# Kernel optimization log

Hardware: AMD Instinct MI355X
Metric: run time of the kernel (lower is better)

## Reference

```python
import jax, jax.numpy as jnp
import numpy as np

INP = 64   # inplanes
PLN = 64   # planes
LOC = 64   # loc_planes
EPS = 1e-5


def _linear_init(key, fan_in, fan_out):
    # torch nn.Linear default: U(-1/sqrt(fan_in), 1/sqrt(fan_in)) for W and b
    kw, kb = jax.random.split(key)
    bound = 1.0 / np.sqrt(fan_in)
    W = jax.random.uniform(kw, (fan_in, fan_out), jnp.float32, -bound, bound)
    b = jax.random.uniform(kb, (fan_out,), jnp.float32, -bound, bound)
    return W, b


def setup_inputs() -> dict:
    key = jax.random.key(0)
    ks = jax.random.split(key, 8)
    B, N = 8, 4096
    img_fea = jax.random.normal(ks[0], (B, N, INP), jnp.float32)
    loc_fea = jax.random.normal(ks[1], (B, N, LOC), jnp.float32)
    W11, b11 = _linear_init(ks[2], INP + LOC, INP)
    W12, b12 = _linear_init(ks[3], INP, INP)
    W21, b21 = _linear_init(ks[4], INP + LOC, INP)
    W22, b22 = _linear_init(ks[5], INP, INP * PLN)
    W3, b3 = _linear_init(ks[6], PLN, PLN)
    ln_g = jnp.ones((PLN,), jnp.float32)
    ln_b = jnp.zeros((PLN,), jnp.float32)
    return {
        "img_fea": img_fea, "loc_fea": loc_fea,
        "W11": W11, "b11": b11, "W12": W12, "b12": b12,
        "W21": W21, "b21": b21, "W22": W22, "b22": b22,
        "ln_g": ln_g, "ln_b": ln_b, "W3": W3, "b3": b3,
    }


def reference(img_fea, loc_fea, W11, b11, W12, b12, W21, b21, W22, b22,
              ln_g, ln_b, W3, b3):
    B, N, C = img_fea.shape
    cat_fea = jnp.concatenate([img_fea, loc_fea], axis=2)  # [B,N,INP+LOC]
    # branch 1: per-token input vector
    w11 = jax.nn.relu(cat_fea @ W11 + b11)                 # [B,N,INP]
    w12 = w11 @ W12 + b12                                  # [B,N,INP]
    # branch 2: per-token weight matrix generation
    w21 = jax.nn.relu(cat_fea @ W21 + b21)                 # [B,N,INP]
    w22 = (w21 @ W22 + b22).reshape(B, N, INP, PLN)        # [B,N,INP,PLN]
    # batched tiny matvec: (1,INP) @ (INP,PLN) per token
    x = jnp.einsum('bni,bnio->bno', w12, w22)              # [B,N,PLN]
    # LayerNorm over last dim + ReLU
    mu = jnp.mean(x, axis=-1, keepdims=True)
    var = jnp.mean(jnp.square(x - mu), axis=-1, keepdims=True)
    x = (x - mu) * jax.lax.rsqrt(var + EPS) * ln_g + ln_b
    x = jax.nn.relu(x)
    # final linear (no activation)
    return x @ W3 + b3
```

## Files before the change

kernel.cpp:

```cpp
#include <hip/hip_runtime.h>
#include <cstdint>


typedef __bf16 bf16x4 __attribute__((ext_vector_type(4)));
typedef __bf16 bf16x8 __attribute__((ext_vector_type(8)));
typedef float  f32x4  __attribute__((ext_vector_type(4)));
typedef float  f32x8  __attribute__((ext_vector_type(8)));

#define MFMA16(A, B, C) __builtin_amdgcn_mfma_f32_16x16x32_bf16(A, B, C, 0, 0, 0)

#define OFF_BT22 0
#define OFF_W11  266240
#define OFF_W21  274432
#define OFF_W12  282624
#define OFF_W3   286720

__global__ __launch_bounds__(256) void prep_kernel(
    const float* __restrict__ W22, const float* __restrict__ b22,
    const float* __restrict__ W11, const float* __restrict__ W21,
    const float* __restrict__ W12, const float* __restrict__ W3,
    __bf16* __restrict__ ws)
{
    __shared__ __bf16 T[64][72];
    const int b = blockIdx.x, tid = threadIdx.x;
    const float* src; __bf16* dst;
    if (b < 64)       { src = W22 + b * 4096;        dst = ws + OFF_BT22 + b * 4096; }
    else if (b == 64) { src = b22;                   dst = ws + OFF_BT22 + 64 * 4096; }
    else if (b < 67)  { src = W11 + (b - 65) * 4096; dst = ws + OFF_W11 + (b - 65) * 4096; }
    else if (b < 69)  { src = W21 + (b - 67) * 4096; dst = ws + OFF_W21 + (b - 67) * 4096; }
    else if (b == 69) { src = W12;                   dst = ws + OFF_W12; }
    else              { src = W3;                    dst = ws + OFF_W3; }
    #pragma unroll
    for (int it = 0; it < 4; ++it) {
        int u = it * 1024 + tid * 4;
        int r = u >> 6, c = u & 63;
        const float4 v = *(const float4*)(src + u);
        T[r][c] = (__bf16)v.x; T[r][c + 1] = (__bf16)v.y;
        T[r][c + 2] = (__bf16)v.z; T[r][c + 3] = (__bf16)v.w;
    }
    __syncthreads();
    #pragma unroll
    for (int it = 0; it < 2; ++it) {
        int item = it * 256 + tid;
        int q = item >> 6, o = item & 63;
        bf16x8 pk;
        #pragma unroll
        for (int kj = 0; kj < 8; ++kj) pk[kj] = T[q * 8 + kj][o];
        *(bf16x8*)(dst + q * 512 + o * 8) = pk;
    }
}

__global__ __launch_bounds__(256, 1) void main_kernel(
    const float* __restrict__ img, const float* __restrict__ loc,
    const float* __restrict__ b11, const float* __restrict__ b12,
    const float* __restrict__ b21, const float* __restrict__ ln_g,
    const float* __restrict__ ln_b, const float* __restrict__ b3,
    const __bf16* __restrict__ ws, float* __restrict__ out)
{
    __shared__ __align__(1024) char smem[102400];
    __bf16* catL = (__bf16*)smem;
    __bf16* w11L = (__bf16*)(smem + 34816);
    __bf16* w21L = (__bf16*)(smem + 65536);
    __bf16* w12L = (__bf16*)(smem + 83968);

    const int tid  = threadIdx.x;
    const int wv   = tid >> 6;
    const int lane = tid & 63;
    const int ln   = lane & 15;
    const int quad = lane >> 4;
    const int wt   = wv * 32;
    const long tb  = (long)blockIdx.x * 128;

    const __bf16* Bt22  = ws + OFF_BT22;
    const __bf16* W11bt = ws + OFF_W11;
    const __bf16* W21bt = ws + OFF_W21;
    const __bf16* W12bt = ws + OFF_W12;
    const __bf16* W3bt  = ws + OFF_W3;

    {
        const float* srcs[2] = {img, loc};
        #pragma unroll
        for (int s = 0; s < 2; ++s) {
            const float* src = srcs[s] + tb * 64;
            #pragma unroll
            for (int it = 0; it < 8; ++it) {
                int u = (it * 256 + tid) * 4;
                int t = u >> 6, c = u & 63;
                const float4 v = *(const float4*)(src + u);
                bf16x4 pk = {(__bf16)v.x, (__bf16)v.y, (__bf16)v.z, (__bf16)v.w};
                *(bf16x4*)(catL + t * 136 + s * 64 + c) = pk;
            }
        }
    }
    __syncthreads();

    {
        f32x4 a11[2][4] = {}; f32x4 a21[2][4] = {};
        #pragma unroll
        for (int kb = 0; kb < 4; ++kb) {
            bf16x8 af[2];
            #pragma unroll
            for (int mf = 0; mf < 2; ++mf)
                af[mf] = *(const bf16x8*)(catL + (wt + mf*16 + ln)*136 + kb*32 + quad*8);
            #pragma unroll
            for (int nf = 0; nf < 4; ++nf) {
                int o = nf*16 + ln;
                bf16x8 bw1 = *(const bf16x8*)(W11bt + ((kb*4 + quad)*64 + o)*8);
                bf16x8 bw2 = *(const bf16x8*)(W21bt + ((kb*4 + quad)*64 + o)*8);
                #pragma unroll
                for (int mf = 0; mf < 2; ++mf) {
                    a11[mf][nf] = MFMA16(af[mf], bw1, a11[mf][nf]);
                    a21[mf][nf] = MFMA16(af[mf], bw2, a21[mf][nf]);
                }
            }
        }
        #pragma unroll
        for (int nf = 0; nf < 4; ++nf) {
            int o = nf*16 + ln;
            float c11 = b11[o], c21 = b21[o];
            #pragma unroll
            for (int mf = 0; mf < 2; ++mf)
                #pragma unroll
                for (int r = 0; r < 4; ++r) {
                    int t = wt + mf*16 + quad*4 + r;
                    float v1 = a11[mf][nf][r] + c11; v1 = v1 > 0.f ? v1 : 0.f;
                    float v2 = a21[mf][nf][r] + c21; v2 = v2 > 0.f ? v2 : 0.f;
                    w11L[t*72 + o] = (__bf16)v1;
                    w21L[t*72 + o] = (__bf16)v2;
                }
        }
    }
    __syncthreads();

    auto stage = [&](int c) {
        const int ng = (c == 16) ? 8 : 32;
        char* buf = smem + (c & 1) * 32768;
        for (int g = wv; g < ng; g += 4) {
            const __bf16* gsrc = Bt22 + ((long)c * 16384 + g * 512) + lane * 8;
            void* ldst = buf + g * 1024;
            __builtin_amdgcn_global_load_lds(
                (const __attribute__((address_space(1))) uint32_t*)gsrc,
                (__attribute__((address_space(3))) uint32_t*)ldst, 16, 0, 0);
        }
    };
    stage(0);

    {
        f32x4 a12c[2][4] = {};
        #pragma unroll
        for (int kb = 0; kb < 2; ++kb) {
            bf16x8 af[2];
            #pragma unroll
            for (int mf = 0; mf < 2; ++mf)
                af[mf] = *(const bf16x8*)(w11L + (wt + mf*16 + ln)*72 + kb*32 + quad*8);
            #pragma unroll
            for (int nf = 0; nf < 4; ++nf) {
                bf16x8 bw = *(const bf16x8*)(W12bt + ((kb*4 + quad)*64 + nf*16 + ln)*8);
                #pragma unroll
                for (int mf = 0; mf < 2; ++mf)
                    a12c[mf][nf] = MFMA16(af[mf], bw, a12c[mf][nf]);
            }
        }
        #pragma unroll
        for (int nf = 0; nf < 4; ++nf) {
            int o = nf*16 + ln;
            float c12 = b12[o];
            #pragma unroll
            for (int mf = 0; mf < 2; ++mf)
                #pragma unroll
                for (int r = 0; r < 4; ++r) {
                    int t = wt + mf*16 + quad*4 + r;
                    w12L[t*72 + o] = (__bf16)(a12c[mf][nf][r] + c12);
                }
        }
    }
    __syncthreads();

    bf16x8 a12[2][2]; f32x8 w12f[2][2];
    #pragma unroll
    for (int mf = 0; mf < 2; ++mf)
        #pragma unroll
        for (int sub = 0; sub < 2; ++sub) {
            a12[mf][sub]  = *(const bf16x8*)(w12L + (wt + mf*16 + ln)*72 + sub*32 + quad*8);
            w12f[mf][sub] = __builtin_convertvector(a12[mf][sub], f32x8);
        }

    f32x4 acc[2][4] = {};
    for (int c = 0; c <= 16; ++c) {
        if (c < 16) stage(c + 1);
        const __bf16* buf = (const __bf16*)(smem + (c & 1) * 32768);
        if (c < 16) {
            bf16x4 w21v[2];
            #pragma unroll
            for (int mf = 0; mf < 2; ++mf)
                w21v[mf] = *(const bf16x4*)(w21L + (wt + mf*16 + ln)*72 + c*4);
            #pragma unroll
            for (int s = 0; s < 8; ++s) {
                int sub = s & 1;
                bf16x8 af[2];
                #pragma unroll
                for (int mf = 0; mf < 2; ++mf) {
                    float wj = (float)w21v[mf][s >> 1];
                    af[mf] = __builtin_convertvector(w12f[mf][sub] * wj, bf16x8);
                }
                #pragma unroll
                for (int nf = 0; nf < 4; ++nf) {
                    bf16x8 bfr = *(const bf16x8*)(buf + (s*4 + quad)*512 + (nf*16 + ln)*8);
                    #pragma unroll
                    for (int mf = 0; mf < 2; ++mf)
                        acc[mf][nf] = MFMA16(af[mf], bfr, acc[mf][nf]);
                }
            }
        } else {
            #pragma unroll
            for (int s = 0; s < 2; ++s)
                #pragma unroll
                for (int nf = 0; nf < 4; ++nf) {
                    bf16x8 bfr = *(const bf16x8*)(buf + (s*4 + quad)*512 + (nf*16 + ln)*8);
                    #pragma unroll
                    for (int mf = 0; mf < 2; ++mf)
                        acc[mf][nf] = MFMA16(a12[mf][s], bfr, acc[mf][nf]);
                }
        }
        __syncthreads();
    }

    float gv[4], bv[4], b3v[4];
    #pragma unroll
    for (int nf = 0; nf < 4; ++nf) {
        int o = nf*16 + ln;
        gv[nf] = ln_g[o]; bv[nf] = ln_b[o]; b3v[nf] = b3[o];
    }
    __bf16* xL = w12L;
    #pragma unroll
    for (int mf = 0; mf < 2; ++mf)
        #pragma unroll
        for (int r = 0; r < 4; ++r) {
            float s1 = 0.f, s2 = 0.f;
            #pragma unroll
            for (int nf = 0; nf < 4; ++nf) { float v = acc[mf][nf][r]; s1 += v; s2 += v*v; }
            #pragma unroll
            for (int d = 1; d < 16; d <<= 1) {
                s1 += __shfl_xor(s1, d, 64);
                s2 += __shfl_xor(s2, d, 64);
            }
            float mean = s1 * 0.015625f;
            float var  = s2 * 0.015625f - mean * mean;
            float inv  = rsqrtf(var + 1e-5f);
            int t = wt + mf*16 + quad*4 + r;
            #pragma unroll
            for (int nf = 0; nf < 4; ++nf) {
                float v = (acc[mf][nf][r] - mean) * inv * gv[nf] + bv[nf];
                v = v > 0.f ? v : 0.f;
                xL[t*72 + nf*16 + ln] = (__bf16)v;
            }
        }
    __syncthreads();

    f32x4 a3[2][4] = {};
    #pragma unroll
    for (int kb = 0; kb < 2; ++kb) {
        bf16x8 af[2];
        #pragma unroll
        for (int mf = 0; mf < 2; ++mf)
            af[mf] = *(const bf16x8*)(xL + (wt + mf*16 + ln)*72 + kb*32 + quad*8);
        #pragma unroll
        for (int nf = 0; nf < 4; ++nf) {
            bf16x8 bfr = *(const bf16x8*)(W3bt + ((kb*4 + quad)*64 + nf*16 + ln)*8);
            #pragma unroll
            for (int mf = 0; mf < 2; ++mf)
                a3[mf][nf] = MFMA16(af[mf], bfr, a3[mf][nf]);
        }
    }
    #pragma unroll
    for (int mf = 0; mf < 2; ++mf)
        #pragma unroll
        for (int nf = 0; nf < 4; ++nf)
            #pragma unroll
            for (int r = 0; r < 4; ++r) {
                long t = tb + wt + mf*16 + quad*4 + r;
                out[t*64 + nf*16 + ln] = a3[mf][nf][r] + b3v[nf];
            }
}

extern "C" void kernel_launch(void* const* d_in, const int* in_sizes, int n_in,
                              void* d_out, int out_size, void* d_ws, size_t ws_size,
                              hipStream_t stream)
{
    const float* img  = (const float*)d_in[0];
    const float* loc  = (const float*)d_in[1];
    const float* W11  = (const float*)d_in[2];
    const float* b11  = (const float*)d_in[3];
    const float* W12  = (const float*)d_in[4];
    const float* b12  = (const float*)d_in[5];
    const float* W21  = (const float*)d_in[6];
    const float* b21  = (const float*)d_in[7];
    const float* W22  = (const float*)d_in[8];
    const float* b22  = (const float*)d_in[9];
    const float* ln_g = (const float*)d_in[10];
    const float* ln_b = (const float*)d_in[11];
    const float* W3   = (const float*)d_in[12];
    const float* b3   = (const float*)d_in[13];
    __bf16* ws = (__bf16*)d_ws;
    float*  o  = (float*)d_out;

    prep_kernel<<<71, 256, 0, stream>>>(W22, b22, W11, W21, W12, W3, ws);
    main_kernel<<<256, 256, 0, stream>>>(img, loc, b11, b12, b21, ln_g, ln_b, b3, ws, o);
}
```

Measured before the change: 133.0 us.

## Split output columns across waves, halve tokens per block, double grid

Each block now handles 64 tokens instead of 128. The four waves form a 2x2 grid over token halves and output-column halves, and the first GEMM is split so half the waves compute W11 and half compute W21. LDS shrinks to 60KB with launch bounds of 2 blocks per CU, and the grid doubles to 512 blocks so the device is better filled and there is more latency hiding. In exchange, the W22 stream is re-read twice as many times in total, since each block still streams all of W22 in smaller 16KB chunks across 32 stages with more barriers, and LayerNorm needs a cross-wave partial-sum exchange through LDS.

```diff
diff --git a/kernel.cpp b/kernel.cpp
--- a/kernel.cpp
+++ b/kernel.cpp
@@ -2,6 +2,7 @@
 #include <cstdint>
 
 
+typedef __bf16 bf16x2 __attribute__((ext_vector_type(2)));
 typedef __bf16 bf16x4 __attribute__((ext_vector_type(4)));
 typedef __bf16 bf16x8 __attribute__((ext_vector_type(8)));
 typedef float  f32x4  __attribute__((ext_vector_type(4)));
@@ -50,26 +51,30 @@
     }
 }
 
-__global__ __launch_bounds__(256, 1) void main_kernel(
+__global__ __launch_bounds__(256, 2) void main_kernel(
     const float* __restrict__ img, const float* __restrict__ loc,
     const float* __restrict__ b11, const float* __restrict__ b12,
     const float* __restrict__ b21, const float* __restrict__ ln_g,
     const float* __restrict__ ln_b, const float* __restrict__ b3,
     const __bf16* __restrict__ ws, float* __restrict__ out)
 {
-    __shared__ __align__(1024) char smem[102400];
+    __shared__ __align__(1024) char smem[61440];
     __bf16* catL = (__bf16*)smem;
-    __bf16* w11L = (__bf16*)(smem + 34816);
-    __bf16* w21L = (__bf16*)(smem + 65536);
-    __bf16* w12L = (__bf16*)(smem + 83968);
+    __bf16* w11L = (__bf16*)(smem + 32768);
+    __bf16* w21L = (__bf16*)(smem + 41984);
+    __bf16* w12L = (__bf16*)(smem + 51200);
+    float2* ps   = (float2*)(smem + 60416);
 
     const int tid  = threadIdx.x;
     const int wv   = tid >> 6;
     const int lane = tid & 63;
     const int ln   = lane & 15;
     const int quad = lane >> 4;
-    const int wt   = wv * 32;
-    const long tb  = (long)blockIdx.x * 128;
+    const int th   = wv & 1;
+    const int oh   = wv >> 1;
+    const int wt   = th * 32;
+    const int ob   = oh * 32;
+    const long tb  = (long)blockIdx.x * 64;
 
     const __bf16* Bt22  = ws + OFF_BT22;
     const __bf16* W11bt = ws + OFF_W11;
@@ -83,7 +88,7 @@
         for (int s = 0; s < 2; ++s) {
             const float* src = srcs[s] + tb * 64;
             #pragma unroll
-            for (int it = 0; it < 8; ++it) {
+            for (int it = 0; it < 4; ++it) {
                 int u = (it * 256 + tid) * 4;
                 int t = u >> 6, c = u & 63;
                 const float4 v = *(const float4*)(src + u);
@@ -95,7 +100,10 @@
     __syncthreads();
 
     {
-        f32x4 a11[2][4] = {}; f32x4 a21[2][4] = {};
+        const __bf16* Wbt = oh ? W21bt : W11bt;
+        const float* bsel = oh ? b21 : b11;
+        __bf16* tgtL      = oh ? w21L : w11L;
+        f32x4 a1[2][4] = {};
         #pragma unroll
         for (int kb = 0; kb < 4; ++kb) {
             bf16x8 af[2];
@@ -104,39 +112,33 @@
                 af[mf] = *(const bf16x8*)(catL + (wt + mf*16 + ln)*136 + kb*32 + quad*8);
             #pragma unroll
             for (int nf = 0; nf < 4; ++nf) {
-                int o = nf*16 + ln;
-                bf16x8 bw1 = *(const bf16x8*)(W11bt + ((kb*4 + quad)*64 + o)*8);
-                bf16x8 bw2 = *(const bf16x8*)(W21bt + ((kb*4 + quad)*64 + o)*8);
-                #pragma unroll
-                for (int mf = 0; mf < 2; ++mf) {
-                    a11[mf][nf] = MFMA16(af[mf], bw1, a11[mf][nf]);
-                    a21[mf][nf] = MFMA16(af[mf], bw2, a21[mf][nf]);
-                }
+                bf16x8 bw = *(const bf16x8*)(Wbt + ((kb*4 + quad)*64 + nf*16 + ln)*8);
+                #pragma unroll
+                for (int mf = 0; mf < 2; ++mf)
+                    a1[mf][nf] = MFMA16(af[mf], bw, a1[mf][nf]);
             }
         }
         #pragma unroll
         for (int nf = 0; nf < 4; ++nf) {
             int o = nf*16 + ln;
-            float c11 = b11[o], c21 = b21[o];
+            float cb = bsel[o];
             #pragma unroll
             for (int mf = 0; mf < 2; ++mf)
                 #pragma unroll
                 for (int r = 0; r < 4; ++r) {
                     int t = wt + mf*16 + quad*4 + r;
-                    float v1 = a11[mf][nf][r] + c11; v1 = v1 > 0.f ? v1 : 0.f;
-                    float v2 = a21[mf][nf][r] + c21; v2 = v2 > 0.f ? v2 : 0.f;
-                    w11L[t*72 + o] = (__bf16)v1;
-                    w21L[t*72 + o] = (__bf16)v2;
+                    float v = a1[mf][nf][r] + cb; v = v > 0.f ? v : 0.f;
+                    tgtL[t*72 + o] = (__bf16)v;
                 }
         }
     }
     __syncthreads();
 
     auto stage = [&](int c) {
-        const int ng = (c == 16) ? 8 : 32;
-        char* buf = smem + (c & 1) * 32768;
+        const int ng = (c == 32) ? 8 : 16;
+        char* buf = smem + (c & 1) * 16384;
         for (int g = wv; g < ng; g += 4) {
-            const __bf16* gsrc = Bt22 + ((long)c * 16384 + g * 512) + lane * 8;
+            const __bf16* gsrc = Bt22 + ((long)c * 8192 + g * 512) + lane * 8;
             void* ldst = buf + g * 1024;
             __builtin_amdgcn_global_load_lds(
                 (const __attribute__((address_space(1))) uint32_t*)gsrc,
@@ -146,7 +148,7 @@
     stage(0);
 
     {
-        f32x4 a12c[2][4] = {};
+        f32x4 a12c[2][2] = {};
         #pragma unroll
         for (int kb = 0; kb < 2; ++kb) {
             bf16x8 af[2];
@@ -154,16 +156,16 @@
             for (int mf = 0; mf < 2; ++mf)
                 af[mf] = *(const bf16x8*)(w11L + (wt + mf*16 + ln)*72 + kb*32 + quad*8);
             #pragma unroll
-            for (int nf = 0; nf < 4; ++nf) {
-                bf16x8 bw = *(const bf16x8*)(W12bt + ((kb*4 + quad)*64 + nf*16 + ln)*8);
+            for (int nf = 0; nf < 2; ++nf) {
+                bf16x8 bw = *(const bf16x8*)(W12bt + ((kb*4 + quad)*64 + ob + nf*16 + ln)*8);
                 #pragma unroll
                 for (int mf = 0; mf < 2; ++mf)
                     a12c[mf][nf] = MFMA16(af[mf], bw, a12c[mf][nf]);
             }
         }
         #pragma unroll
-        for (int nf = 0; nf < 4; ++nf) {
-            int o = nf*16 + ln;
+        for (int nf = 0; nf < 2; ++nf) {
+            int o = ob + nf*16 + ln;
             float c12 = b12[o];
             #pragma unroll
             for (int mf = 0; mf < 2; ++mf)
@@ -185,17 +187,17 @@
             w12f[mf][sub] = __builtin_convertvector(a12[mf][sub], f32x8);
         }
 
-    f32x4 acc[2][4] = {};
-    for (int c = 0; c <= 16; ++c) {
-        if (c < 16) stage(c + 1);
-        const __bf16* buf = (const __bf16*)(smem + (c & 1) * 32768);
-        if (c < 16) {
-            bf16x4 w21v[2];
-            #pragma unroll
-            for (int mf = 0; mf < 2; ++mf)
-                w21v[mf] = *(const bf16x4*)(w21L + (wt + mf*16 + ln)*72 + c*4);
-            #pragma unroll
-            for (int s = 0; s < 8; ++s) {
+    f32x4 acc[2][2] = {};
+    for (int c = 0; c <= 32; ++c) {
+        if (c < 32) stage(c + 1);
+        const __bf16* buf = (const __bf16*)(smem + (c & 1) * 16384);
+        if (c < 32) {
+            bf16x2 w21v[2];
+            #pragma unroll
+            for (int mf = 0; mf < 2; ++mf)
+                w21v[mf] = *(const bf16x2*)(w21L + (wt + mf*16 + ln)*72 + c*2);
+            #pragma unroll
+            for (int s = 0; s < 4; ++s) {
                 int sub = s & 1;
                 bf16x8 af[2];
                 #pragma unroll
@@ -204,8 +206,8 @@
                     af[mf] = __builtin_convertvector(w12f[mf][sub] * wj, bf16x8);
                 }
                 #pragma unroll
-                for (int nf = 0; nf < 4; ++nf) {
-                    bf16x8 bfr = *(const bf16x8*)(buf + (s*4 + quad)*512 + (nf*16 + ln)*8);
+                for (int nf = 0; nf < 2; ++nf) {
+                    bf16x8 bfr = *(const bf16x8*)(buf + (s*4 + quad)*512 + (ob + nf*16 + ln)*8);
                     #pragma unroll
                     for (int mf = 0; mf < 2; ++mf)
                         acc[mf][nf] = MFMA16(af[mf], bfr, acc[mf][nf]);
@@ -215,8 +217,8 @@
             #pragma unroll
             for (int s = 0; s < 2; ++s)
                 #pragma unroll
-                for (int nf = 0; nf < 4; ++nf) {
-                    bf16x8 bfr = *(const bf16x8*)(buf + (s*4 + quad)*512 + (nf*16 + ln)*8);
+                for (int nf = 0; nf < 2; ++nf) {
+                    bf16x8 bfr = *(const bf16x8*)(buf + (s*4 + quad)*512 + (ob + nf*16 + ln)*8);
                     #pragma unroll
                     for (int mf = 0; mf < 2; ++mf)
                         acc[mf][nf] = MFMA16(a12[mf][s], bfr, acc[mf][nf]);
@@ -225,39 +227,51 @@
         __syncthreads();
     }
 
-    float gv[4], bv[4], b3v[4];
-    #pragma unroll
-    for (int nf = 0; nf < 4; ++nf) {
-        int o = nf*16 + ln;
-        gv[nf] = ln_g[o]; bv[nf] = ln_b[o]; b3v[nf] = b3[o];
-    }
-    __bf16* xL = w12L;
     #pragma unroll
     for (int mf = 0; mf < 2; ++mf)
         #pragma unroll
         for (int r = 0; r < 4; ++r) {
             float s1 = 0.f, s2 = 0.f;
             #pragma unroll
-            for (int nf = 0; nf < 4; ++nf) { float v = acc[mf][nf][r]; s1 += v; s2 += v*v; }
+            for (int nf = 0; nf < 2; ++nf) { float v = acc[mf][nf][r]; s1 += v; s2 += v*v; }
             #pragma unroll
             for (int d = 1; d < 16; d <<= 1) {
                 s1 += __shfl_xor(s1, d, 64);
                 s2 += __shfl_xor(s2, d, 64);
             }
-            float mean = s1 * 0.015625f;
-            float var  = s2 * 0.015625f - mean * mean;
+            if (ln == 0) {
+                int t = wt + mf*16 + quad*4 + r;
+                ps[t*2 + oh] = make_float2(s1, s2);
+            }
+        }
+    __syncthreads();
+
+    float gv[2], bv[2], b3v[2];
+    #pragma unroll
+    for (int nf = 0; nf < 2; ++nf) {
+        int o = ob + nf*16 + ln;
+        gv[nf] = ln_g[o]; bv[nf] = ln_b[o]; b3v[nf] = b3[o];
+    }
+    __bf16* xL = w12L;
+    #pragma unroll
+    for (int mf = 0; mf < 2; ++mf)
+        #pragma unroll
+        for (int r = 0; r < 4; ++r) {
+            int t = wt + mf*16 + quad*4 + r;
+            float2 p0 = ps[t*2], p1 = ps[t*2 + 1];
+            float mean = (p0.x + p1.x) * 0.015625f;
+            float var  = (p0.y + p1.y) * 0.015625f - mean * mean;
             float inv  = rsqrtf(var + 1e-5f);
-            int t = wt + mf*16 + quad*4 + r;
-            #pragma unroll
-            for (int nf = 0; nf < 4; ++nf) {
+            #pragma unroll
+            for (int nf = 0; nf < 2; ++nf) {
                 float v = (acc[mf][nf][r] - mean) * inv * gv[nf] + bv[nf];
                 v = v > 0.f ? v : 0.f;
-                xL[t*72 + nf*16 + ln] = (__bf16)v;
-            }
-        }
-    __syncthreads();
-
-    f32x4 a3[2][4] = {};
+                xL[t*72 + ob + nf*16 + ln] = (__bf16)v;
+            }
+        }
+    __syncthreads();
+
+    f32x4 a3[2][2] = {};
     #pragma unroll
     for (int kb = 0; kb < 2; ++kb) {
         bf16x8 af[2];
@@ -265,8 +279,8 @@
         for (int mf = 0; mf < 2; ++mf)
             af[mf] = *(const bf16x8*)(xL + (wt + mf*16 + ln)*72 + kb*32 + quad*8);
         #pragma unroll
-        for (int nf = 0; nf < 4; ++nf) {
-            bf16x8 bfr = *(const bf16x8*)(W3bt + ((kb*4 + quad)*64 + nf*16 + ln)*8);
+        for (int nf = 0; nf < 2; ++nf) {
+            bf16x8 bfr = *(const bf16x8*)(W3bt + ((kb*4 + quad)*64 + ob + nf*16 + ln)*8);
             #pragma unroll
             for (int mf = 0; mf < 2; ++mf)
                 a3[mf][nf] = MFMA16(af[mf], bfr, a3[mf][nf]);
@@ -275,11 +289,11 @@
     #pragma unroll
     for (int mf = 0; mf < 2; ++mf)
         #pragma unroll
-        for (int nf = 0; nf < 4; ++nf)
+        for (int nf = 0; nf < 2; ++nf)
             #pragma unroll
             for (int r = 0; r < 4; ++r) {
                 long t = tb + wt + mf*16 + quad*4 + r;
-                out[t*64 + nf*16 + ln] = a3[mf][nf][r] + b3v[nf];
+                out[t*64 + ob + nf*16 + ln] = a3[mf][nf][r] + b3v[nf];
             }
 }
 
@@ -305,5 +319,5 @@
     float*  o  = (float*)d_out;
 
     prep_kernel<<<71, 256, 0, stream>>>(W22, b22, W11, W21, W12, W3, ws);
-    main_kernel<<<256, 256, 0, stream>>>(img, loc, b11, b12, b21, ln_g, ln_b, b3, ws, o);
+    main_kernel<<<512, 256, 0, stream>>>(img, loc, b11, b12, b21, ln_g, ln_b, b3, ws, o);
 }
```

Result: faster. 128.4 us (-3.5%).
